# Optimization experiments

Hardware: AMD Instinct MI355X
Metric: run time of the kernel (lower is better)

## Reference

```python
import jax, jax.numpy as jnp
import numpy as np

B = 2048
PARAM_SHAPES = {
    'l1c0': (1, 8, 3, 3), 'l1c1': (3, 4, 8, 2), 'l1c2': (2, 4, 8, 2), 'l1c3': (2, 4, 8, 2), 'l1c4': (2, 4, 8, 1), 'b1': (8, 4, 4, 4, 4),
    'l2c0': (1, 4, 8, 2), 'l2c1': (2, 2, 4, 2), 'l2c2': (2, 2, 4, 2), 'l2c3': (2, 2, 4, 2), 'l2c4': (2, 2, 4, 1), 'b2': (4, 2, 2, 2, 2),
    'l3c0': (1, 2, 4, 2), 'l3c1': (2, 2, 2, 2), 'l3c2': (2, 2, 2, 2), 'l3c3': (2, 2, 2, 2), 'l3c4': (2, 2, 2, 1), 'b3': (2, 2, 2, 2, 2),
    'W': (2, 32), 'bl': (2,),
}

def setup_inputs():
    key = jax.random.key(0)
    ks = jax.random.split(key, len(PARAM_SHAPES) + 1)
    inp = {'x': jax.random.normal(ks[0], (B, 3, 8, 8, 8, 8), dtype=jnp.float32)}
    for k, (name, shp) in zip(ks[1:], PARAM_SHAPES.items()):
        scale = 0.5 if name[0] == 'l' and name != 'bl' else 0.1
        inp[name] = jax.random.normal(k, shp, dtype=jnp.float32) * scale
    return inp

def tt_linear(x, cores, bias):
    # y[b, m1..md] = sum_{n1..nd} W[m1..md, n1..nd] x[b, n1..nd] + bias[m1..md]
    # W is the TT-matrix with cores G_k of shape (r_{k-1}, m_k, n_k, r_k).
    b = x.shape[0]
    z = x.reshape(b, 1, -1)  # (B, rank, flat=[n_k..n_d, m_1..m_{k-1}])
    for G in cores:
        r0, m, n, r1 = G.shape
        z = jnp.einsum('brns,rmnq->bqsm', z.reshape(b, r0, n, -1), G).reshape(b, r1, -1)
    return z.reshape((b,) + bias.shape) + bias

def reference(x, l1c0, l1c1, l1c2, l1c3, l1c4, b1, l2c0, l2c1, l2c2, l2c3, l2c4, b2, l3c0, l3c1, l3c2, l3c3, l3c4, b3, W, bl):
    h = jax.nn.relu(tt_linear(x, [l1c0, l1c1, l1c2, l1c3, l1c4], b1))
    h = jax.nn.relu(tt_linear(h, [l2c0, l2c1, l2c2, l2c3, l2c4], b2))
    h = jax.nn.relu(tt_linear(h, [l3c0, l3c1, l3c2, l3c3, l3c4], b3))
    logits = h.reshape(-1, 32) @ W.T + bl  # (B, 2)
    return jax.nn.log_softmax(logits, axis=1)
```

## Files before the change

kernel.cpp:

```cpp
#include <hip/hip_runtime.h>
#include <math.h>

#define WC3   0
#define WC2   128
#define WU1   256
#define T2S0  288
#define T2S1  1440
#define T3S   2592
#define H1O   288
#define BO    2336
#define CO    3488
#define DO    4032
#define H2O   4304
#define H3O   4368
#define LDS_FLOATS 4400

__global__ void tt_setup_w3(const float* __restrict__ v0, const float* __restrict__ v1,
                            const float* __restrict__ v2, const float* __restrict__ v3,
                            const float* __restrict__ v4, float* __restrict__ w3) {
    int i = blockIdx.x * 256 + threadIdx.x;
    if (i >= 2048) return;
    int mi = i >> 6, nj = i & 63;
    int m1 = (mi >> 4) & 1, m2 = (mi >> 3) & 1, m3 = (mi >> 2) & 1, m4 = (mi >> 1) & 1, m5 = mi & 1;
    int n1 = (nj >> 4) & 3, n2 = (nj >> 3) & 1, n3 = (nj >> 2) & 1, n4 = (nj >> 1) & 1, n5 = nj & 1;
    float s = 0.f;
#pragma unroll
    for (int q1 = 0; q1 < 2; ++q1) {
        float a1 = v0[(m1 * 4 + n1) * 2 + q1];
#pragma unroll
        for (int q2 = 0; q2 < 2; ++q2) {
            float a2 = a1 * v1[((q1 * 2 + m2) * 2 + n2) * 2 + q2];
#pragma unroll
            for (int q3 = 0; q3 < 2; ++q3) {
                float a3 = a2 * v2[((q2 * 2 + m3) * 2 + n3) * 2 + q3];
#pragma unroll
                for (int q4 = 0; q4 < 2; ++q4)
                    s = fmaf(a3 * v3[((q3 * 2 + m4) * 2 + n4) * 2 + q4],
                             v4[(q4 * 2 + m5) * 2 + n5], s);
            }
        }
    }
    w3[i] = s;
}

__global__ __launch_bounds__(128)
__attribute__((amdgpu_waves_per_eu(4, 4)))
void tt_main(const float* __restrict__ x,
             const float* __restrict__ g0, const float* __restrict__ g1,
             const float* __restrict__ g2, const float* __restrict__ g3,
             const float* __restrict__ g4, const float* __restrict__ b1g,
             const float* __restrict__ u0, const float* __restrict__ u1,
             const float* __restrict__ u2, const float* __restrict__ u3,
             const float* __restrict__ u4, const float* __restrict__ b2g,
             const float* __restrict__ b3g,
             const float* __restrict__ Wmg, const float* __restrict__ blg,
             const float* __restrict__ w3g,
             float* __restrict__ out)
{
    __shared__ float smem[LDS_FLOATS];
    const int t   = threadIdx.x;
    const int tl  = t & 63;
    const int wid = t >> 6;
    const int b = blockIdx.x;
    const float* xb = x + (size_t)b * 12288;

    float xv[32];
    {
        const float4* xq = (const float4*)xb + wid * 512 + tl * 8;
#pragma unroll
        for (int i = 0; i < 8; ++i) {
            const float4 v = xq[i];
            xv[i*4+0] = v.x; xv[i*4+1] = v.y; xv[i*4+2] = v.z; xv[i*4+3] = v.w;
        }
    }

    smem[WC3 + t] = g3[t];
    smem[WC2 + t] = g2[t];
    if (t < 32) smem[WU1 + t] = u1[t];
    __syncthreads();

    const int h = tl & 1;
    const int p = tl >> 1;
    const int T2W = wid ? T2S1 : T2S0;

    float regT4[18];
#pragma unroll
    for (int i = 0; i < 18; ++i) regT4[i] = 0.f;

#pragma unroll
    for (int n1 = 0; n1 < 3; ++n1) {
        float t1[32];
#pragma unroll
        for (int m5 = 0; m5 < 4; ++m5)
#pragma unroll
        for (int q4 = 0; q4 < 2; ++q4) {
            const float* w = g4 + (q4 * 4 + m5) * 8;
#pragma unroll
            for (int n4l = 0; n4l < 4; ++n4l) {
                float sa = xv[n4l*8+0] * w[0];
#pragma unroll
                for (int n5 = 1; n5 < 8; ++n5) sa = fmaf(xv[n4l*8+n5], w[n5], sa);
                t1[n4l*8 + m5*2 + q4] = sa;
            }
        }

        if (n1 < 2) {
            const float4* xq = (const float4*)xb + ((n1 + 1) * 2 + wid) * 512 + tl * 8;
#pragma unroll
            for (int i = 0; i < 8; ++i) {
                const float4 v = xq[i];
                xv[i*4+0] = v.x; xv[i*4+1] = v.y; xv[i*4+2] = v.z; xv[i*4+3] = v.w;
            }
        }

        float acc[16];
#pragma unroll
        for (int i = 0; i < 16; ++i) acc[i] = 0.f;
#pragma unroll
        for (int pass = 0; pass < 2; ++pass) {
            const int hh = (pass == 0) ? h : (1 - h);
            if (pass == 1) {
#pragma unroll
                for (int i = 0; i < 32; ++i) t1[i] = __shfl_xor(t1[i], 1);
            }
#pragma unroll
            for (int m4 = 0; m4 < 4; ++m4) {
                const int cbase = WC3 + ((h * 4 + m4) * 8 + hh * 4) * 2;
                const float4 c0 = *(const float4*)&smem[cbase];
                const float4 c1 = *(const float4*)&smem[cbase + 4];
                const float cs[8] = {c0.x, c0.y, c0.z, c0.w, c1.x, c1.y, c1.z, c1.w};
#pragma unroll
                for (int m5 = 0; m5 < 4; ++m5) {
                    float sa = acc[m4*4+m5];
#pragma unroll
                    for (int n4l = 0; n4l < 4; ++n4l)
#pragma unroll
                    for (int q4 = 0; q4 < 2; ++q4)
                        sa = fmaf(t1[n4l*8 + m5*2 + q4], cs[n4l*2 + q4], sa);
                    acc[m4*4+m5] = sa;
                }
            }
        }

        asm volatile("" ::: "memory");
#pragma unroll
        for (int m45 = 0; m45 < 16; ++m45)
            smem[T2W + p * 36 + m45 * 2 + h] = acc[m45];
        asm volatile("" ::: "memory");

        {
            const int n3h = tl & 1;
            const int q2  = (tl >> 1) & 1;
            const int m3  = (tl >> 2) & 3;
            const int n2l = tl >> 4;
            float o3[16];
#pragma unroll
            for (int i = 0; i < 16; ++i) o3[i] = 0.f;
#pragma unroll
            for (int n3l = 0; n3l < 4; ++n3l) {
                const int rb = T2W + (n2l * 8 + n3h * 4 + n3l) * 36;
                float rv[32];
#pragma unroll
                for (int g = 0; g < 8; ++g) {
                    const float4 v = *(const float4*)&smem[rb + g * 4];
                    rv[g*4+0] = v.x; rv[g*4+1] = v.y; rv[g*4+2] = v.z; rv[g*4+3] = v.w;
                }
                const int wb = WC2 + ((q2 * 4 + m3) * 8 + n3h * 4 + n3l) * 2;
                const float w0 = smem[wb], w1 = smem[wb + 1];
#pragma unroll
                for (int m45 = 0; m45 < 16; ++m45)
                    o3[m45] = fmaf(rv[m45*2], w0, fmaf(rv[m45*2+1], w1, o3[m45]));
            }
#pragma unroll
            for (int k = 0; k < 16; ++k) o3[k] += __shfl_xor(o3[k], 1);
            const int row = wid * 16 + n2l * 4 + m3;
#pragma unroll
            for (int k = 0; k < 8; ++k) {
                const float v = n3h ? o3[8 + k] : o3[k];
                smem[T3S + row * 34 + (n3h * 8 + k) * 2 + q2] = v;
            }
        }
        __syncthreads();

        {
            const int m3 = tl >> 4, m4 = (tl >> 2) & 3, m5 = tl & 3;
            float2 zz[8];
#pragma unroll
            for (int n2 = 0; n2 < 8; ++n2)
                zz[n2] = *(const float2*)&smem[T3S + (n2 * 4 + m3) * 34 + (m4 * 4 + m5) * 2];
#pragma unroll
            for (int j = 0; j < 2; ++j) {
                const int jj = wid * 2 + j;
#pragma unroll
                for (int q1 = 0; q1 < 3; ++q1) {
                    float sa = regT4[j * 9 + n1 * 3 + q1];
#pragma unroll
                    for (int n2g = 0; n2g < 4; ++n2g) {
                        const float4 w = *(const float4*)(g1 + ((q1 * 4 + jj) * 8 + n2g * 2) * 2);
                        sa = fmaf(zz[n2g*2].x,   w.x, sa);
                        sa = fmaf(zz[n2g*2].y,   w.y, sa);
                        sa = fmaf(zz[n2g*2+1].x, w.z, sa);
                        sa = fmaf(zz[n2g*2+1].y, w.w, sa);
                    }
                    regT4[j * 9 + n1 * 3 + q1] = sa;
                }
            }
        }
        __syncthreads();
    }

#pragma unroll
    for (int j = 0; j < 2; ++j) {
        const int jj = wid * 2 + j;
        float bia[8];
#pragma unroll
        for (int m1 = 0; m1 < 8; ++m1) bia[m1] = b1g[m1 * 256 + jj * 64 + tl];
#pragma unroll
        for (int m1 = 0; m1 < 8; ++m1) {
            float sa = bia[m1];
#pragma unroll
            for (int n1 = 0; n1 < 3; ++n1)
#pragma unroll
            for (int q1 = 0; q1 < 3; ++q1)
                sa = fmaf(regT4[j * 9 + n1 * 3 + q1], g0[(m1 * 3 + n1) * 3 + q1], sa);
            smem[H1O + m1 * 256 + jj * 64 + tl] = fmaxf(sa, 0.f);
        }
    }
    __syncthreads();

#pragma unroll
    for (int pp = 0; pp < 4; ++pp) {
        const int P = pp * 128 + t;
        float4* ap = (float4*)&smem[H1O + P * 4];
        const float4 hv = *ap;
        float4 av;
        av.x = hv.x*u4[0]  + hv.y*u4[1]  + hv.z*u4[2]  + hv.w*u4[3];
        av.y = hv.x*u4[8]  + hv.y*u4[9]  + hv.z*u4[10] + hv.w*u4[11];
        av.z = hv.x*u4[4]  + hv.y*u4[5]  + hv.z*u4[6]  + hv.w*u4[7];
        av.w = hv.x*u4[12] + hv.y*u4[13] + hv.z*u4[14] + hv.w*u4[15];
        *ap = av;
    }
    __syncthreads();

    {
        float4 aa[4];
#pragma unroll
        for (int n4 = 0; n4 < 4; ++n4)
            aa[n4] = *(const float4*)&smem[H1O + (t * 4 + n4) * 4];
        float o[8];
#pragma unroll
        for (int i = 0; i < 8; ++i) o[i] = 0.f;
#pragma unroll
        for (int n4 = 0; n4 < 4; ++n4)
#pragma unroll
        for (int q4 = 0; q4 < 2; ++q4) {
            const float a0 = q4 ? aa[n4].y : aa[n4].x;
            const float a1 = q4 ? aa[n4].w : aa[n4].z;
#pragma unroll
            for (int q3 = 0; q3 < 2; ++q3)
#pragma unroll
            for (int m4 = 0; m4 < 2; ++m4) {
                const float w = u3[((q3 * 2 + m4) * 4 + n4) * 2 + q4];
                o[(m4 * 2 + 0) * 2 + q3] = fmaf(a0, w, o[(m4 * 2 + 0) * 2 + q3]);
                o[(m4 * 2 + 1) * 2 + q3] = fmaf(a1, w, o[(m4 * 2 + 1) * 2 + q3]);
            }
        }
#pragma unroll
        for (int k = 0; k < 8; ++k) smem[BO + t * 9 + k] = o[k];
    }
    __syncthreads();

    if (t < 32) {
        float o[16];
#pragma unroll
        for (int i = 0; i < 16; ++i) o[i] = 0.f;
#pragma unroll
        for (int n3 = 0; n3 < 4; ++n3)
#pragma unroll
        for (int q3 = 0; q3 < 2; ++q3) {
            float zb[4];
#pragma unroll
            for (int m45 = 0; m45 < 4; ++m45)
                zb[m45] = smem[BO + (t * 4 + n3) * 9 + m45 * 2 + q3];
#pragma unroll
            for (int m3 = 0; m3 < 2; ++m3)
#pragma unroll
            for (int q2 = 0; q2 < 2; ++q2) {
                const float w = u2[((q2 * 2 + m3) * 4 + n3) * 2 + q3];
#pragma unroll
                for (int m45 = 0; m45 < 4; ++m45)
                    o[(m3 * 4 + m45) * 2 + q2] = fmaf(zb[m45], w, o[(m3 * 4 + m45) * 2 + q2]);
            }
        }
#pragma unroll
        for (int k = 0; k < 16; ++k) smem[CO + t * 17 + k] = o[k];
    }
    __syncthreads();

    if (t < 32) {
        const int n1 = t >> 2, m2 = (t >> 1) & 1, m3 = t & 1;
        float o[8];
#pragma unroll
        for (int i = 0; i < 8; ++i) o[i] = 0.f;
#pragma unroll
        for (int n2 = 0; n2 < 4; ++n2)
#pragma unroll
        for (int q2 = 0; q2 < 2; ++q2) {
            float cb[4];
#pragma unroll
            for (int m45 = 0; m45 < 4; ++m45)
                cb[m45] = smem[CO + (n1 * 4 + n2) * 17 + (m3 * 4 + m45) * 2 + q2];
#pragma unroll
            for (int q1 = 0; q1 < 2; ++q1) {
                const float w = smem[WU1 + ((q1 * 2 + m2) * 4 + n2) * 2 + q2];
#pragma unroll
                for (int m45 = 0; m45 < 4; ++m45)
                    o[m45 * 2 + q1] = fmaf(cb[m45], w, o[m45 * 2 + q1]);
            }
        }
#pragma unroll
        for (int m45 = 0; m45 < 4; ++m45)
#pragma unroll
        for (int q1 = 0; q1 < 2; ++q1)
            smem[DO + (m2 * 8 + m3 * 4 + m45) * 17 + n1 * 2 + q1] = o[m45 * 2 + q1];
    }
    __syncthreads();

    if (t < 16) {
        float o[4];
#pragma unroll
        for (int i = 0; i < 4; ++i) o[i] = 0.f;
#pragma unroll
        for (int n1 = 0; n1 < 8; ++n1)
#pragma unroll
        for (int q1 = 0; q1 < 2; ++q1) {
            const float dv = smem[DO + t * 17 + n1 * 2 + q1];
#pragma unroll
            for (int m1 = 0; m1 < 4; ++m1)
                o[m1] = fmaf(dv, u0[(m1 * 8 + n1) * 2 + q1], o[m1]);
        }
#pragma unroll
        for (int m1 = 0; m1 < 4; ++m1)
            smem[H2O + m1 * 16 + t] = fmaxf(o[m1] + b2g[m1 * 16 + t], 0.f);
    }
    __syncthreads();

    if (t < 32) {
        const float4* wr = (const float4*)(w3g + t * 64);
        float sa = b3g[t];
#pragma unroll
        for (int g = 0; g < 16; ++g) {
            const float4 w4 = wr[g];
            sa = fmaf(w4.x, smem[H2O + g*4 + 0],
                 fmaf(w4.y, smem[H2O + g*4 + 1],
                 fmaf(w4.z, smem[H2O + g*4 + 2],
                 fmaf(w4.w, smem[H2O + g*4 + 3], sa))));
        }
        smem[H3O + t] = fmaxf(sa, 0.f);
    }
    __syncthreads();

    if (t < 64) {
        const int k = t & 31;
        float pr = smem[H3O + k] * Wmg[t];
#pragma unroll
        for (int d = 16; d >= 1; d >>= 1) pr += __shfl_xor(pr, d);
        const float l0 = __shfl(pr, 0) + blg[0];
        const float l1 = __shfl(pr, 32) + blg[1];
        if (t == 0) {
            const float mm = fmaxf(l0, l1);
            const float lse = mm + logf(expf(l0 - mm) + expf(l1 - mm));
            out[(size_t)b * 2 + 0] = l0 - lse;
            out[(size_t)b * 2 + 1] = l1 - lse;
        }
    }
}

extern "C" void kernel_launch(void* const* d_in, const int* in_sizes, int n_in,
                              void* d_out, int out_size, void* d_ws, size_t ws_size,
                              hipStream_t stream) {
    const float* x    = (const float*)d_in[0];
    const float* l1c0 = (const float*)d_in[1];
    const float* l1c1 = (const float*)d_in[2];
    const float* l1c2 = (const float*)d_in[3];
    const float* l1c3 = (const float*)d_in[4];
    const float* l1c4 = (const float*)d_in[5];
    const float* b1   = (const float*)d_in[6];
    const float* l2c0 = (const float*)d_in[7];
    const float* l2c1 = (const float*)d_in[8];
    const float* l2c2 = (const float*)d_in[9];
    const float* l2c3 = (const float*)d_in[10];
    const float* l2c4 = (const float*)d_in[11];
    const float* b2   = (const float*)d_in[12];
    const float* l3c0 = (const float*)d_in[13];
    const float* l3c1 = (const float*)d_in[14];
    const float* l3c2 = (const float*)d_in[15];
    const float* l3c3 = (const float*)d_in[16];
    const float* l3c4 = (const float*)d_in[17];
    const float* b3   = (const float*)d_in[18];
    const float* Wm   = (const float*)d_in[19];
    const float* bl   = (const float*)d_in[20];
    float* W3 = (float*)d_ws;

    tt_setup_w3<<<8, 256, 0, stream>>>(l3c0, l3c1, l3c2, l3c3, l3c4, W3);
    tt_main<<<2048, 128, 0, stream>>>(x, l1c0, l1c1, l1c2, l1c3, l1c4, b1,
                                      l2c0, l2c1, l2c2, l2c3, l2c4, b2, b3,
                                      Wm, bl, W3, (float*)d_out);
}
```

Before: 215.2 us.

## Keep per-wave partial sums to remove per-iteration block barriers

Each wave now computes partial contributions for all four output groups from its own half of the n2 range, keeping intermediates in its private LDS region. This removes the two __syncthreads per n1 iteration. Partials are exchanged through LDS once at the end with a single barrier pair. The cost is doubling the regT4 accumulator registers, so the occupancy hint is relaxed from exactly 4 waves to at least 3 waves per EU.

```diff
diff --git a/kernel.cpp b/kernel.cpp
--- a/kernel.cpp
+++ b/kernel.cpp
@@ -4,9 +4,8 @@
 #define WC3   0
 #define WC2   128
 #define WU1   256
-#define T2S0  288
-#define T2S1  1440
-#define T3S   2592
+#define Z0    288
+#define Z1    1440
 #define H1O   288
 #define BO    2336
 #define CO    3488
@@ -44,7 +43,7 @@
 }
 
 __global__ __launch_bounds__(128)
-__attribute__((amdgpu_waves_per_eu(4, 4)))
+__attribute__((amdgpu_waves_per_eu(3)))
 void tt_main(const float* __restrict__ x,
              const float* __restrict__ g0, const float* __restrict__ g1,
              const float* __restrict__ g2, const float* __restrict__ g3,
@@ -81,11 +80,11 @@
 
     const int h = tl & 1;
     const int p = tl >> 1;
-    const int T2W = wid ? T2S1 : T2S0;
-
-    float regT4[18];
-#pragma unroll
-    for (int i = 0; i < 18; ++i) regT4[i] = 0.f;
+    const int ZW = wid ? Z1 : Z0;
+
+    float regT4[36];
+#pragma unroll
+    for (int i = 0; i < 36; ++i) regT4[i] = 0.f;
 
 #pragma unroll
     for (int n1 = 0; n1 < 3; ++n1) {
@@ -145,7 +144,7 @@
         asm volatile("" ::: "memory");
 #pragma unroll
         for (int m45 = 0; m45 < 16; ++m45)
-            smem[T2W + p * 36 + m45 * 2 + h] = acc[m45];
+            smem[ZW + p * 36 + m45 * 2 + h] = acc[m45];
         asm volatile("" ::: "memory");
 
         {
@@ -158,7 +157,7 @@
             for (int i = 0; i < 16; ++i) o3[i] = 0.f;
 #pragma unroll
             for (int n3l = 0; n3l < 4; ++n3l) {
-                const int rb = T2W + (n2l * 8 + n3h * 4 + n3l) * 36;
+                const int rb = ZW + (n2l * 8 + n3h * 4 + n3l) * 36;
                 float rv[32];
 #pragma unroll
                 for (int g = 0; g < 8; ++g) {
@@ -173,56 +172,83 @@
             }
 #pragma unroll
             for (int k = 0; k < 16; ++k) o3[k] += __shfl_xor(o3[k], 1);
-            const int row = wid * 16 + n2l * 4 + m3;
+            asm volatile("" ::: "memory");
+            const int row = n2l * 4 + m3;
 #pragma unroll
             for (int k = 0; k < 8; ++k) {
                 const float v = n3h ? o3[8 + k] : o3[k];
-                smem[T3S + row * 34 + (n3h * 8 + k) * 2 + q2] = v;
-            }
-        }
-        __syncthreads();
+                smem[ZW + row * 34 + (n3h * 8 + k) * 2 + q2] = v;
+            }
+            asm volatile("" ::: "memory");
+        }
 
         {
             const int m3 = tl >> 4, m4 = (tl >> 2) & 3, m5 = tl & 3;
-            float2 zz[8];
-#pragma unroll
-            for (int n2 = 0; n2 < 8; ++n2)
-                zz[n2] = *(const float2*)&smem[T3S + (n2 * 4 + m3) * 34 + (m4 * 4 + m5) * 2];
-#pragma unroll
-            for (int j = 0; j < 2; ++j) {
-                const int jj = wid * 2 + j;
-#pragma unroll
-                for (int q1 = 0; q1 < 3; ++q1) {
-                    float sa = regT4[j * 9 + n1 * 3 + q1];
-#pragma unroll
-                    for (int n2g = 0; n2g < 4; ++n2g) {
-                        const float4 w = *(const float4*)(g1 + ((q1 * 4 + jj) * 8 + n2g * 2) * 2);
-                        sa = fmaf(zz[n2g*2].x,   w.x, sa);
-                        sa = fmaf(zz[n2g*2].y,   w.y, sa);
-                        sa = fmaf(zz[n2g*2+1].x, w.z, sa);
-                        sa = fmaf(zz[n2g*2+1].y, w.w, sa);
-                    }
-                    regT4[j * 9 + n1 * 3 + q1] = sa;
+            float2 zz[4];
+#pragma unroll
+            for (int l = 0; l < 4; ++l)
+                zz[l] = *(const float2*)&smem[ZW + (l * 4 + m3) * 34 + (m4 * 4 + m5) * 2];
+#pragma unroll
+            for (int jj = 0; jj < 4; ++jj)
+#pragma unroll
+            for (int q1 = 0; q1 < 3; ++q1) {
+                float sa = regT4[jj * 9 + n1 * 3 + q1];
+#pragma unroll
+                for (int g = 0; g < 2; ++g) {
+                    const float4 w = *(const float4*)(g1 + ((q1 * 4 + jj) * 8 + wid * 4 + g * 2) * 2);
+                    sa = fmaf(zz[g*2].x,   w.x, sa);
+                    sa = fmaf(zz[g*2].y,   w.y, sa);
+                    sa = fmaf(zz[g*2+1].x, w.z, sa);
+                    sa = fmaf(zz[g*2+1].y, w.w, sa);
                 }
-            }
-        }
-        __syncthreads();
-    }
-
+                regT4[jj * 9 + n1 * 3 + q1] = sa;
+            }
+        }
+        asm volatile("" ::: "memory");
+    }
+
+    float bia[2][8];
 #pragma unroll
     for (int j = 0; j < 2; ++j) {
         const int jj = wid * 2 + j;
-        float bia[8];
-#pragma unroll
-        for (int m1 = 0; m1 < 8; ++m1) bia[m1] = b1g[m1 * 256 + jj * 64 + tl];
+#pragma unroll
+        for (int m1 = 0; m1 < 8; ++m1) bia[j][m1] = b1g[m1 * 256 + jj * 64 + tl];
+    }
+
+    {
+        const int pbase = (1 - wid) * 18;
+        asm volatile("" ::: "memory");
+#pragma unroll
+        for (int kk = 0; kk < 9; ++kk) {
+            float2 v; v.x = regT4[pbase + 2*kk]; v.y = regT4[pbase + 2*kk + 1];
+            *(float2*)&smem[ZW + tl * 18 + 2 * kk] = v;
+        }
+    }
+    __syncthreads();
+    {
+        const int ZP = wid ? Z0 : Z1;
+        const int obase = wid * 18;
+#pragma unroll
+        for (int kk = 0; kk < 9; ++kk) {
+            const float2 v = *(const float2*)&smem[ZP + tl * 18 + 2 * kk];
+            regT4[obase + 2*kk]     += v.x;
+            regT4[obase + 2*kk + 1] += v.y;
+        }
+    }
+    __syncthreads();
+
+#pragma unroll
+    for (int j = 0; j < 2; ++j) {
+        const int jj = wid * 2 + j;
+        const int rb = (wid * 2 + j) * 9;
 #pragma unroll
         for (int m1 = 0; m1 < 8; ++m1) {
-            float sa = bia[m1];
+            float sa = bia[j][m1];
 #pragma unroll
             for (int n1 = 0; n1 < 3; ++n1)
 #pragma unroll
             for (int q1 = 0; q1 < 3; ++q1)
-                sa = fmaf(regT4[j * 9 + n1 * 3 + q1], g0[(m1 * 3 + n1) * 3 + q1], sa);
+                sa = fmaf(regT4[rb + n1 * 3 + q1], g0[(m1 * 3 + n1) * 3 + q1], sa);
             smem[H1O + m1 * 256 + jj * 64 + tl] = fmaxf(sa, 0.f);
         }
     }
```

Measured after the change: 240.9 us. 11.9% more time.
